# Kernel optimization log

Hardware: AMD Instinct MI355X
Metric: run time of the kernel (lower is better)

Reference implementation:

```python
import jax, jax.numpy as jnp
import numpy as np

NUM_STATES = 32768
NUM_LABELS = 64
BATCH = 512


def setup_inputs() -> dict:
    key = jax.random.key(0)
    k1, k2, k3, k4 = jax.random.split(key, 4)
    f = jax.random.normal(k1, (BATCH, NUM_LABELS), dtype=jnp.float32)
    # legal_state: binary indicator matrix [num_states, num_labels]
    S = jax.random.randint(k2, (NUM_STATES, NUM_LABELS), 0, 2).astype(jnp.float32)
    y = jax.random.uniform(k3, (BATCH, NUM_LABELS), dtype=jnp.float32)
    mask = jax.random.randint(k4, (BATCH, NUM_LABELS), 0, 2).astype(jnp.float32)
    return {"f": f, "S": S, "y": y, "mask": mask}


def reference(f, S, y, mask):
    # potential[s, b] = sum_i S[s, i] * f[b, i]
    potential = jnp.einsum('si,bi->sb', S, f)
    # stable softmax over the state axis (replaces exp/max/sum in original)
    P = jax.nn.softmax(potential, axis=0)  # [num_states, batch]
    # pMargin[b, i] = sum_{s: S[s,i]>0} P[s, b]  ->  indicator-matrix GEMM
    pMargin = jnp.einsum('sb,si->bi', P, S)  # [batch, num_labels]
    # per-column BCE (torch BCELoss clamps log at -100), masked, mean over batch
    logp = jnp.clip(jnp.log(pMargin), -100.0, None)
    log1mp = jnp.clip(jnp.log(1.0 - pMargin), -100.0, None)
    bce = -(y * logp + (1.0 - y) * log1mp) * mask  # [batch, num_labels]
    loss = jnp.sum(jnp.mean(bce, axis=0))  # sum over columns of per-column means
    return loss, pMargin
```

## Files before the change

### kernel.cpp

```cpp
#include <hip/hip_runtime.h>
#include <hip/hip_bf16.h>
#include <math.h>

#define N_STATES 32768
#define N_LABELS 64
#define N_BATCH  512

#define ZP_F     1024
#define UP_F     65536

typedef __attribute__((ext_vector_type(8))) short bfrag;
typedef __attribute__((ext_vector_type(4))) float f32x4;

static __device__ __forceinline__ unsigned short f2bf(float x) {
    __hip_bfloat16 h = __float2bfloat16(x);
    return *reinterpret_cast<unsigned short*>(&h);
}
static __device__ __forceinline__ float bf2f(unsigned short u) {
    __hip_bfloat16 h;
    *reinterpret_cast<unsigned short*>(&h) = u;
    return __bfloat162float(h);
}

__global__ __launch_bounds__(256, 2) void fused_kernel(
    const float* __restrict__ f, const float* __restrict__ S,
    float* __restrict__ ws, float* __restrict__ out) {
    __shared__ alignas(16) unsigned char smem[66560];

    const int t     = threadIdx.x;
    const int lane  = t & 63;
    const int w     = t >> 6;
    const int x     = lane & 15;
    const int quad  = lane >> 4;
    const int btile = blockIdx.x >> 6;
    const int chunk = blockIdx.x & 63;

    bfrag fh[4][2], fl[4][2];
    float Mv[4];
    #pragma unroll
    for (int nt = 0; nt < 4; nt++) {
        const float4* fp = reinterpret_cast<const float4*>(
            f + ((size_t)(btile * 64 + nt * 16 + x)) * N_LABELS);
        float msum = 0.f;
        #pragma unroll
        for (int kh = 0; kh < 2; kh++) {
            float4 a = fp[kh * 8 + quad * 2];
            float4 b = fp[kh * 8 + quad * 2 + 1];
            float vv[8] = {a.x,a.y,a.z,a.w, b.x,b.y,b.z,b.w};
            #pragma unroll
            for (int j = 0; j < 8; j++) {
                msum += fmaxf(vv[j], 0.f);
                unsigned short h = f2bf(vv[j]);
                fh[nt][kh][j] = (short)h;
                fl[nt][kh][j] = (short)f2bf(vv[j] - bf2f(h));
            }
        }
        msum += __shfl_xor(msum, 16, 64);
        msum += __shfl_xor(msum, 32, 64);
        Mv[nt] = msum;
    }

    f32x4 Uacc[16];
    #pragma unroll
    for (int e = 0; e < 16; e++) Uacc[e] = (f32x4){0.f, 0.f, 0.f, 0.f};
    float zacc[4] = {0.f, 0.f, 0.f, 0.f};

    #pragma unroll
    for (int st = 0; st < 8; st++) {
        const int s0 = (chunk * 8 + st) * 64;

        const float* Arow = S + (size_t)(s0 + 16 * w + x) * N_LABELS + quad * 8;
        float4 r0 = *(const float4*)(Arow);
        float4 r1 = *(const float4*)(Arow + 4);
        float4 r2 = *(const float4*)(Arow + 32);
        float4 r3 = *(const float4*)(Arow + 36);
        bfrag a0 = {(short)f2bf(r0.x), (short)f2bf(r0.y), (short)f2bf(r0.z), (short)f2bf(r0.w),
                    (short)f2bf(r1.x), (short)f2bf(r1.y), (short)f2bf(r1.z), (short)f2bf(r1.w)};
        bfrag a1 = {(short)f2bf(r2.x), (short)f2bf(r2.y), (short)f2bf(r2.z), (short)f2bf(r2.w),
                    (short)f2bf(r3.x), (short)f2bf(r3.y), (short)f2bf(r3.z), (short)f2bf(r3.w)};

        const float* Acol = S + (size_t)(s0 + 16 * w + 4 * quad) * N_LABELS + x;
        bfrag A8[4];
        #pragma unroll
        for (int it = 0; it < 4; it++) {
            float c0 = Acol[0 * 64 + it * 16];
            float c1 = Acol[1 * 64 + it * 16];
            float c2 = Acol[2 * 64 + it * 16];
            float c3 = Acol[3 * 64 + it * 16];
            bfrag tmp = {(short)f2bf(c0), (short)f2bf(c1),
                         (short)f2bf(c2), (short)f2bf(c3), 0, 0, 0, 0};
            A8[it] = tmp;
        }

        #pragma unroll
        for (int nt = 0; nt < 4; nt++) {
            f32x4 acc = (f32x4){0.f, 0.f, 0.f, 0.f};
            acc = __builtin_amdgcn_mfma_f32_16x16x32_bf16(a0, fh[nt][0], acc, 0, 0, 0);
            acc = __builtin_amdgcn_mfma_f32_16x16x32_bf16(a1, fh[nt][1], acc, 0, 0, 0);
            acc = __builtin_amdgcn_mfma_f32_16x16x32_bf16(a0, fl[nt][0], acc, 0, 0, 0);
            acc = __builtin_amdgcn_mfma_f32_16x16x32_bf16(a1, fl[nt][1], acc, 0, 0, 0);
            float e0 = __expf(acc[0] - Mv[nt]);
            float e1 = __expf(acc[1] - Mv[nt]);
            float e2 = __expf(acc[2] - Mv[nt]);
            float e3 = __expf(acc[3] - Mv[nt]);
            zacc[nt] += (e0 + e1) + (e2 + e3);
            bfrag Bf = {(short)f2bf(e0), (short)f2bf(e1),
                        (short)f2bf(e2), (short)f2bf(e3), 0, 0, 0, 0};
            #pragma unroll
            for (int it = 0; it < 4; it++)
                Uacc[it * 4 + nt] =
                    __builtin_amdgcn_mfma_f32_16x16x32_bf16(A8[it], Bf, Uacc[it * 4 + nt], 0, 0, 0);
        }
    }

    float* mg  = (float*)smem;
    float* zsh = (float*)(smem + 65536);
    #pragma unroll
    for (int e = 0; e < 16; e++) {
        #pragma unroll
        for (int r = 0; r < 4; r++)
            mg[w * 4096 + (e * 4 + r) * 64 + lane] = Uacc[e][r];
    }
    #pragma unroll
    for (int nt = 0; nt < 4; nt++) {
        float v = zacc[nt];
        v += __shfl_down(v, 32, 64);
        v += __shfl_down(v, 16, 64);
        if (quad == 0) zsh[w * 64 + nt * 16 + x] = v;
    }
    __syncthreads();

    float* Up = ws + UP_F;
    #pragma unroll
    for (int k = 0; k < 16; k++) {
        int idx = k * 256 + t;
        int e  = idx >> 6;
        int ln = idx & 63;
        int it = e >> 4, nt = (e >> 2) & 3, r = e & 3;
        int i  = it * 16 + (ln >> 4) * 4 + r;
        int b  = nt * 16 + (ln & 15);
        float s = mg[idx] + mg[4096 + idx] + mg[8192 + idx] + mg[12288 + idx];
        Up[((btile * 64 + i) * 64 + chunk) * 64 + b] = s;
    }
    if (t < 64) {
        float z = zsh[t] + zsh[64 + t] + zsh[128 + t] + zsh[192 + t];
        (ws + ZP_F)[(btile * 64 + chunk) * 64 + t] = z;
    }
    if (blockIdx.x == 0 && t == 0) out[0] = 0.f;
}

__global__ __launch_bounds__(256) void finalize_kernel(
    const float* __restrict__ ws, const float* __restrict__ y,
    const float* __restrict__ mask, float* __restrict__ out) {
    const int i     = blockIdx.x >> 1;
    const int b     = ((blockIdx.x & 1) << 8) + threadIdx.x;
    const int btile = b >> 6;
    const int bl    = b & 63;

    const float* zp = ws + ZP_F + (btile * 64) * 64 + bl;
    const float* up = ws + UP_F + ((btile * 64 + i) * 64) * 64 + bl;
    float z = 0.f, u = 0.f;
    #pragma unroll 8
    for (int c = 0; c < 64; c++) { z += zp[c * 64]; u += up[c * 64]; }

    float p = fminf(fmaxf(u / z, 0.f), 1.f);
    const int idx = b * 64 + i;
    out[1 + idx] = p;

    float lp  = fmaxf(logf(p), -100.f);
    float l1p = fmaxf(logf(1.f - p), -100.f);
    float yy = y[idx];
    float bce = -(yy * lp + (1.f - yy) * l1p) * mask[idx] * (1.f / (float)N_BATCH);

    float v = bce;
    #pragma unroll
    for (int off = 32; off > 0; off >>= 1) v += __shfl_down(v, off, 64);
    __shared__ float wsum[4];
    if ((threadIdx.x & 63) == 0) wsum[threadIdx.x >> 6] = v;
    __syncthreads();
    if (threadIdx.x == 0)
        atomicAdd(&out[0], wsum[0] + wsum[1] + wsum[2] + wsum[3]);
}

extern "C" void kernel_launch(void* const* d_in, const int* in_sizes, int n_in,
                              void* d_out, int out_size, void* d_ws, size_t ws_size,
                              hipStream_t stream) {
    const float* f    = (const float*)d_in[0];
    const float* S    = (const float*)d_in[1];
    const float* y    = (const float*)d_in[2];
    const float* mask = (const float*)d_in[3];
    float* out = (float*)d_out;
    float* ws  = (float*)d_ws;

    fused_kernel<<<512, 256, 0, stream>>>(f, S, ws, out);
    finalize_kernel<<<128, 256, 0, stream>>>(ws, y, mask, out);
}
```

Measured before the change: 96.23 us.

## Drop bf16 split-precision f, double chunk grid, shrink LDS staging

Result: slower. 130.2 us (+35.3%).

```diff
diff --git a/kernel.cpp b/kernel.cpp
--- a/kernel.cpp
+++ b/kernel.cpp
@@ -5,37 +5,40 @@
 #define N_STATES 32768
 #define N_LABELS 64
 #define N_BATCH  512
+#define N_CHUNKS 128
 
 #define ZP_F     1024
-#define UP_F     65536
+#define UP_F     131072
 
 typedef __attribute__((ext_vector_type(8))) short bfrag;
 typedef __attribute__((ext_vector_type(4))) float f32x4;
 
+#define PSEL 0x07060302u
+static __device__ __forceinline__ unsigned pk2(float hi, float lo) {
+    return __builtin_amdgcn_perm(__float_as_uint(hi), __float_as_uint(lo), PSEL);
+}
 static __device__ __forceinline__ unsigned short f2bf(float x) {
     __hip_bfloat16 h = __float2bfloat16(x);
     return *reinterpret_cast<unsigned short*>(&h);
 }
-static __device__ __forceinline__ float bf2f(unsigned short u) {
-    __hip_bfloat16 h;
-    *reinterpret_cast<unsigned short*>(&h) = u;
-    return __bfloat162float(h);
-}
-
-__global__ __launch_bounds__(256, 2) void fused_kernel(
+
+union frag_u { bfrag v; unsigned u[4]; };
+
+__global__ __launch_bounds__(256, 3) void fused_kernel(
     const float* __restrict__ f, const float* __restrict__ S,
     float* __restrict__ ws, float* __restrict__ out) {
-    __shared__ alignas(16) unsigned char smem[66560];
+    __shared__ float mg[4 * 2048];
+    __shared__ float zshm[256];
 
     const int t     = threadIdx.x;
     const int lane  = t & 63;
     const int w     = t >> 6;
     const int x     = lane & 15;
     const int quad  = lane >> 4;
-    const int btile = blockIdx.x >> 6;
-    const int chunk = blockIdx.x & 63;
-
-    bfrag fh[4][2], fl[4][2];
+    const int btile = blockIdx.x >> 7;
+    const int chunk = blockIdx.x & 127;
+
+    bfrag fh[4][2];
     float Mv[4];
     #pragma unroll
     for (int nt = 0; nt < 4; nt++) {
@@ -50,9 +53,7 @@
             #pragma unroll
             for (int j = 0; j < 8; j++) {
                 msum += fmaxf(vv[j], 0.f);
-                unsigned short h = f2bf(vv[j]);
-                fh[nt][kh][j] = (short)h;
-                fl[nt][kh][j] = (short)f2bf(vv[j] - bf2f(h));
+                fh[nt][kh][j] = (short)f2bf(vv[j]);
             }
         }
         msum += __shfl_xor(msum, 16, 64);
@@ -66,85 +67,91 @@
     float zacc[4] = {0.f, 0.f, 0.f, 0.f};
 
     #pragma unroll
-    for (int st = 0; st < 8; st++) {
-        const int s0 = (chunk * 8 + st) * 64;
+    for (int st = 0; st < 4; st++) {
+        const int s0 = (chunk * 4 + st) * 64;
 
         const float* Arow = S + (size_t)(s0 + 16 * w + x) * N_LABELS + quad * 8;
         float4 r0 = *(const float4*)(Arow);
         float4 r1 = *(const float4*)(Arow + 4);
         float4 r2 = *(const float4*)(Arow + 32);
         float4 r3 = *(const float4*)(Arow + 36);
-        bfrag a0 = {(short)f2bf(r0.x), (short)f2bf(r0.y), (short)f2bf(r0.z), (short)f2bf(r0.w),
-                    (short)f2bf(r1.x), (short)f2bf(r1.y), (short)f2bf(r1.z), (short)f2bf(r1.w)};
-        bfrag a1 = {(short)f2bf(r2.x), (short)f2bf(r2.y), (short)f2bf(r2.z), (short)f2bf(r2.w),
-                    (short)f2bf(r3.x), (short)f2bf(r3.y), (short)f2bf(r3.z), (short)f2bf(r3.w)};
+        frag_u a0, a1;
+        a0.u[0] = pk2(r0.y, r0.x); a0.u[1] = pk2(r0.w, r0.z);
+        a0.u[2] = pk2(r1.y, r1.x); a0.u[3] = pk2(r1.w, r1.z);
+        a1.u[0] = pk2(r2.y, r2.x); a1.u[1] = pk2(r2.w, r2.z);
+        a1.u[2] = pk2(r3.y, r3.x); a1.u[3] = pk2(r3.w, r3.z);
 
         const float* Acol = S + (size_t)(s0 + 16 * w + 4 * quad) * N_LABELS + x;
-        bfrag A8[4];
+        frag_u A8[4];
         #pragma unroll
         for (int it = 0; it < 4; it++) {
             float c0 = Acol[0 * 64 + it * 16];
             float c1 = Acol[1 * 64 + it * 16];
             float c2 = Acol[2 * 64 + it * 16];
             float c3 = Acol[3 * 64 + it * 16];
-            bfrag tmp = {(short)f2bf(c0), (short)f2bf(c1),
-                         (short)f2bf(c2), (short)f2bf(c3), 0, 0, 0, 0};
-            A8[it] = tmp;
+            A8[it].u[0] = pk2(c1, c0);
+            A8[it].u[1] = pk2(c3, c2);
+            A8[it].u[2] = 0; A8[it].u[3] = 0;
         }
 
         #pragma unroll
         for (int nt = 0; nt < 4; nt++) {
             f32x4 acc = (f32x4){0.f, 0.f, 0.f, 0.f};
-            acc = __builtin_amdgcn_mfma_f32_16x16x32_bf16(a0, fh[nt][0], acc, 0, 0, 0);
-            acc = __builtin_amdgcn_mfma_f32_16x16x32_bf16(a1, fh[nt][1], acc, 0, 0, 0);
-            acc = __builtin_amdgcn_mfma_f32_16x16x32_bf16(a0, fl[nt][0], acc, 0, 0, 0);
-            acc = __builtin_amdgcn_mfma_f32_16x16x32_bf16(a1, fl[nt][1], acc, 0, 0, 0);
+            acc = __builtin_amdgcn_mfma_f32_16x16x32_bf16(a0.v, fh[nt][0], acc, 0, 0, 0);
+            acc = __builtin_amdgcn_mfma_f32_16x16x32_bf16(a1.v, fh[nt][1], acc, 0, 0, 0);
             float e0 = __expf(acc[0] - Mv[nt]);
             float e1 = __expf(acc[1] - Mv[nt]);
             float e2 = __expf(acc[2] - Mv[nt]);
             float e3 = __expf(acc[3] - Mv[nt]);
             zacc[nt] += (e0 + e1) + (e2 + e3);
-            bfrag Bf = {(short)f2bf(e0), (short)f2bf(e1),
-                        (short)f2bf(e2), (short)f2bf(e3), 0, 0, 0, 0};
+            frag_u Bf;
+            Bf.u[0] = pk2(e1, e0);
+            Bf.u[1] = pk2(e3, e2);
+            Bf.u[2] = 0; Bf.u[3] = 0;
             #pragma unroll
             for (int it = 0; it < 4; it++)
                 Uacc[it * 4 + nt] =
-                    __builtin_amdgcn_mfma_f32_16x16x32_bf16(A8[it], Bf, Uacc[it * 4 + nt], 0, 0, 0);
-        }
-    }
-
-    float* mg  = (float*)smem;
-    float* zsh = (float*)(smem + 65536);
-    #pragma unroll
-    for (int e = 0; e < 16; e++) {
-        #pragma unroll
-        for (int r = 0; r < 4; r++)
-            mg[w * 4096 + (e * 4 + r) * 64 + lane] = Uacc[e][r];
-    }
+                    __builtin_amdgcn_mfma_f32_16x16x32_bf16(A8[it].v, Bf.v, Uacc[it * 4 + nt], 0, 0, 0);
+        }
+    }
+
     #pragma unroll
     for (int nt = 0; nt < 4; nt++) {
         float v = zacc[nt];
         v += __shfl_down(v, 32, 64);
         v += __shfl_down(v, 16, 64);
-        if (quad == 0) zsh[w * 64 + nt * 16 + x] = v;
-    }
-    __syncthreads();
+        if (quad == 0) zshm[w * 64 + nt * 16 + x] = v;
+    }
 
     float* Up = ws + UP_F;
     #pragma unroll
-    for (int k = 0; k < 16; k++) {
-        int idx = k * 256 + t;
-        int e  = idx >> 6;
-        int ln = idx & 63;
-        int it = e >> 4, nt = (e >> 2) & 3, r = e & 3;
-        int i  = it * 16 + (ln >> 4) * 4 + r;
-        int b  = nt * 16 + (ln & 15);
-        float s = mg[idx] + mg[4096 + idx] + mg[8192 + idx] + mg[12288 + idx];
-        Up[((btile * 64 + i) * 64 + chunk) * 64 + b] = s;
+    for (int pass = 0; pass < 2; pass++) {
+        if (pass) __syncthreads();
+        #pragma unroll
+        for (int el = 0; el < 8; el++) {
+            int e = pass * 8 + el;
+            #pragma unroll
+            for (int r = 0; r < 4; r++)
+                mg[w * 2048 + (el * 4 + r) * 64 + lane] = Uacc[e][r];
+        }
+        __syncthreads();
+        #pragma unroll
+        for (int k = 0; k < 8; k++) {
+            int idx  = k * 256 + t;
+            int slot = idx >> 6;
+            int ln   = idx & 63;
+            int el   = slot >> 2, r = slot & 3;
+            int it   = pass * 2 + (el >> 2);
+            int nt   = el & 3;
+            int i    = it * 16 + (ln >> 4) * 4 + r;
+            int b    = nt * 16 + (ln & 15);
+            float s = mg[idx] + mg[2048 + idx] + mg[4096 + idx] + mg[6144 + idx];
+            Up[((size_t)(btile * 64 + i) * N_CHUNKS + chunk) * 64 + b] = s;
+        }
     }
     if (t < 64) {
-        float z = zsh[t] + zsh[64 + t] + zsh[128 + t] + zsh[192 + t];
-        (ws + ZP_F)[(btile * 64 + chunk) * 64 + t] = z;
+        float z = zshm[t] + zshm[64 + t] + zshm[128 + t] + zshm[192 + t];
+        (ws + ZP_F)[(btile * N_CHUNKS + chunk) * 64 + t] = z;
     }
     if (blockIdx.x == 0 && t == 0) out[0] = 0.f;
 }
@@ -157,11 +164,11 @@
     const int btile = b >> 6;
     const int bl    = b & 63;
 
-    const float* zp = ws + ZP_F + (btile * 64) * 64 + bl;
-    const float* up = ws + UP_F + ((btile * 64 + i) * 64) * 64 + bl;
+    const float* zp = ws + ZP_F + (size_t)(btile * N_CHUNKS) * 64 + bl;
+    const float* up = ws + UP_F + ((size_t)(btile * 64 + i) * N_CHUNKS) * 64 + bl;
     float z = 0.f, u = 0.f;
     #pragma unroll 8
-    for (int c = 0; c < 64; c++) { z += zp[c * 64]; u += up[c * 64]; }
+    for (int c = 0; c < N_CHUNKS; c++) { z += zp[c * 64]; u += up[c * 64]; }
 
     float p = fminf(fmaxf(u / z, 0.f), 1.f);
     const int idx = b * 64 + i;
@@ -192,6 +199,6 @@
     float* out = (float*)d_out;
     float* ws  = (float*)d_ws;
 
-    fused_kernel<<<512, 256, 0, stream>>>(f, S, ws, out);
+    fused_kernel<<<1024, 256, 0, stream>>>(f, S, ws, out);
     finalize_kernel<<<128, 256, 0, stream>>>(ws, y, mask, out);
 }
```
